# Kernel tuning notes

Measured on AMD Instinct MI355X. Metric: run time of the kernel, lower is better.

The kernel has to match this reference:

```python
import jax, jax.numpy as jnp
import numpy as np

N = 100000   # nodes
MUL = 128    # multiplicity of each irrep (128x0e + 128x1o)
NA = 10      # number of scalar node attributes (one-hot elements, 10x0e)
DIM = MUL * 4  # 128 scalars + 128 vectors*3
LIN_SCALE = 1.0 / np.sqrt(MUL)       # e3nn Linear 'element' path norm: 1/sqrt(fan_in)
TP_SCALE = 1.0 / np.sqrt(MUL * NA)   # FCTP single path per l: 1/sqrt(mul_in*mul_attr)


def setup_inputs() -> dict:
    key = jax.random.key(0)
    ks = jax.random.split(key, 7)
    m_i = jax.random.normal(ks[0], (N, DIM), dtype=jnp.float32)
    node_feats = jax.random.normal(ks[1], (N, DIM), dtype=jnp.float32)
    z = jax.random.randint(ks[2], (N,), 0, NA)
    node_attrs = jax.nn.one_hot(z, NA, dtype=jnp.float32)  # 10x0e one-hot element attrs
    Wl0 = jax.random.normal(ks[3], (MUL, MUL), dtype=jnp.float32)       # Linear weight, 0e block
    Wl1 = jax.random.normal(ks[4], (MUL, MUL), dtype=jnp.float32)       # Linear weight, 1o block
    Wt0 = jax.random.normal(ks[5], (MUL, NA, MUL), dtype=jnp.float32)   # FCTP path weight 0e(x)0e->0e
    Wt1 = jax.random.normal(ks[6], (MUL, NA, MUL), dtype=jnp.float32)   # FCTP path weight 1o(x)0e->1o
    return dict(m_i=m_i, node_feats=node_feats, node_attrs=node_attrs,
                Wl0=Wl0, Wl1=Wl1, Wt0=Wt0, Wt1=Wt1)


def _split(x):
    # [N, 512] -> scalars [N,128], vectors [N,128,3]
    return x[:, :MUL], x[:, MUL:].reshape(-1, MUL, 3)


def _forward(m_i, node_feats, node_attrs, Wl0, Wl1, Wt0, Wt1):
    # equivariant Linear on m_i: block-diagonal per-irrep matmul
    ms, mv = _split(m_i)
    lin_s = (ms @ Wl0) * LIN_SCALE                                  # [N,128]
    lin_v = jnp.einsum('nix,io->nox', mv, Wl1) * LIN_SCALE          # [N,128,3]
    # FullyConnectedTensorProduct(node_feats, node_attrs): attrs are 0e scalars,
    # CG l(x)0e->l is identity; per-attr 128x128 path weight. Loop over the 10
    # attribute channels (small fixed set) to avoid a huge [N,128,128] intermediate.
    fs, fv = _split(node_feats)
    res_s = jnp.zeros_like(lin_s)
    res_v = jnp.zeros_like(lin_v)
    for a in range(NA):
        att = node_attrs[:, a]
        res_s = res_s + att[:, None] * (fs @ Wt0[:, a, :])
        res_v = res_v + att[:, None, None] * jnp.einsum('nix,io->nox', fv, Wt1[:, a, :])
    out_s = lin_s + res_s * TP_SCALE
    out_v = lin_v + res_v * TP_SCALE
    return jnp.concatenate([out_s, out_v.reshape(-1, MUL * 3)], axis=1)  # [N,512]


def reference(m_i, node_feats, node_attrs, Wl0, Wl1, Wt0, Wt1):
    return _forward(m_i, node_feats, node_attrs, Wl0, Wl1, Wt0, Wt1)
```

## Files before the change

kernel.cpp:

```cpp
#include <hip/hip_runtime.h>
#include <stdint.h>

#define NA 10
#define DIM 512
#define LIN_SCALE 0.08838834764831845f
#define TP_SCALE  0.027950849718747374f

#define PLANE_SZ 655360
#define CHUNK_SZ 8192

typedef __attribute__((ext_vector_type(8))) short short8;
typedef __attribute__((ext_vector_type(8))) __bf16 bf16x8;
typedef __attribute__((ext_vector_type(4))) float f32x4;
typedef __attribute__((ext_vector_type(4))) float float4v;

static __device__ __forceinline__ unsigned short f2bf(float x) {
  unsigned int u = __float_as_uint(x);
  u += 0x7fffu + ((u >> 16) & 1u);
  return (unsigned short)(u >> 16);
}
static __device__ __forceinline__ float bf2f(unsigned short h) {
  return __uint_as_float(((unsigned int)h) << 16);
}

#define MFMA_BF16(A, B, C) __builtin_amdgcn_mfma_f32_16x16x32_bf16( \
    __builtin_bit_cast(bf16x8, (A)), __builtin_bit_cast(bf16x8, (B)), (C), 0, 0, 0)

__global__ void k_zero(int* wsI) {
  if (threadIdx.x < 48) wsI[threadIdx.x] = 0;
}

__global__ __launch_bounds__(256) void k_count(const float* __restrict__ attrs,
                                               int* wsI, int N) {
  __shared__ int h[16];
  int t = threadIdx.x;
  int n = blockIdx.x * 256 + t;
  if (t < 16) h[t] = 0;
  __syncthreads();
  if (n < N) {
    int a = 0;
    #pragma unroll
    for (int j = 1; j < NA; ++j) if (attrs[n * NA + j] > 0.5f) a = j;
    atomicAdd(&h[a], 1);
  }
  __syncthreads();
  if (t < NA && h[t] > 0) atomicAdd(&wsI[t], h[t]);
}

__global__ void k_scan(int* wsI) {
  if (threadIdx.x == 0) {
    int run = 0;
    for (int a = 0; a < NA; ++a) {
      wsI[16 + a] = run;
      wsI[32 + a] = run;
      run += wsI[a];
    }
  }
}

__global__ __launch_bounds__(256) void k_scatter(const float* __restrict__ attrs,
                                                 int* wsI, int N) {
  __shared__ int h[16], base[16], c2[16];
  int t = threadIdx.x;
  int n = blockIdx.x * 256 + t;
  if (t < 16) { h[t] = 0; c2[t] = 0; }
  __syncthreads();
  int a = 0;
  if (n < N) {
    #pragma unroll
    for (int j = 1; j < NA; ++j) if (attrs[n * NA + j] > 0.5f) a = j;
    atomicAdd(&h[a], 1);
  }
  __syncthreads();
  if (t < NA && h[t] > 0) base[t] = atomicAdd(&wsI[32 + t], h[t]);
  __syncthreads();
  if (n < N) {
    int r = atomicAdd(&c2[a], 1);
    wsI[64 + base[a] + r] = n;
  }
}

__global__ __launch_bounds__(256) void k_prep(const float* __restrict__ Wl0,
                                              const float* __restrict__ Wl1,
                                              const float* __restrict__ Wt0,
                                              const float* __restrict__ Wt1,
                                              char* __restrict__ wb) {
  int gid = blockIdx.x * 256 + threadIdx.x;
  int l  = gid & 63;
  int nb = (gid >> 6) & 7;
  int c  = (gid >> 9) & 7;
  int ac = gid >> 12;
  int a  = ac % NA;
  int type = ac / NA;
  const float* Wl = type ? Wl1 : Wl0;
  const float* Wt = type ? Wt1 : Wt0;
  char* bh = wb + (size_t)type * (2 * (size_t)PLANE_SZ);
  char* bl = bh + PLANE_SZ;
  size_t slot = ((size_t)((a * 8 + c) * 8 + nb) * 64 + l) * 16;
  short8 h8, l8;
  #pragma unroll
  for (int e = 0; e < 8; ++e) {
    int k = c * 32 + (e >> 2) * 16 + (l >> 4) * 4 + (e & 3);
    int n = nb * 16 + (l & 15);
    float w = (k < 128) ? (LIN_SCALE * Wl[k * 128 + n])
                        : (TP_SCALE * Wt[(size_t)(k - 128) * (NA * 128) + a * 128 + n]);
    unsigned short hb = f2bf(w);
    h8[e] = (short)hb;
    l8[e] = (short)f2bf(w - bf2f(hb));
  }
  *(short8*)(bh + slot) = h8;
  *(short8*)(bl + slot) = l8;
}

__global__ __launch_bounds__(256, 2) void k_gemm(const float* __restrict__ m_i,
                                                 const float* __restrict__ feats,
                                                 const int* __restrict__ wsI,
                                                 const char* __restrict__ wb,
                                                 float* __restrict__ out) {
  __shared__ __attribute__((aligned(16))) short Ah[16][64][8];
  __shared__ __attribute__((aligned(16))) short Al[16][64][8];
  __shared__ int nidx[64];

  const int a  = blockIdx.y;
  const int t0 = blockIdx.x * 64;
  const int ca = wsI[a];
  if (t0 >= ca) return;
  const int nn = (ca - t0 < 64) ? (ca - t0) : 64;
  const int tid = threadIdx.x;
  if (tid < 64) nidx[tid] = (tid < nn) ? wsI[64 + wsI[16 + a] + t0 + tid] : 0;

  const int wid  = tid >> 6;
  const int lane = tid & 63;
  const int nd   = tid >> 2;
  const int w    = tid & 3;

  const char* bp_h = wb + (size_t)(wid ? 2 : 0) * PLANE_SZ + (size_t)a * (8 * CHUNK_SZ);
  const char* bp_l = bp_h + PLANE_SZ;

  f32x4 acc[4][8];
  #pragma unroll
  for (int i = 0; i < 4; ++i)
    #pragma unroll
    for (int nbv = 0; nbv < 8; ++nbv)
      acc[i][nbv] = (f32x4){0.f, 0.f, 0.f, 0.f};

  for (int c = 0; c < 8; ++c) {
    __syncthreads();
    {
      const float* src = (c < 4) ? m_i : feats;
      const int cc = c & 3;
      const float* row = src + (size_t)nidx[nd] * DIM;
      const bool ok = (nd < nn);
      {
        float4v f0 = {0,0,0,0}, f1 = {0,0,0,0};
        if (ok) {
          f0 = *(const float4v*)(row + cc * 32 + 4 * w);
          f1 = *(const float4v*)(row + cc * 32 + 16 + 4 * w);
        }
        short8 h8, l8;
        #pragma unroll
        for (int j = 0; j < 4; ++j) {
          unsigned short hb = f2bf(f0[j]);
          h8[j] = (short)hb; l8[j] = (short)f2bf(f0[j] - bf2f(hb));
          unsigned short hb2 = f2bf(f1[j]);
          h8[4 + j] = (short)hb2; l8[4 + j] = (short)f2bf(f1[j] - bf2f(hb2));
        }
        const int rb = nd >> 4, ln = (nd & 15) + 16 * w;
        *(short8*)&Ah[rb][ln][0] = h8;
        *(short8*)&Al[rb][ln][0] = l8;
      }
      {
        const int vb = 128 + cc * 96 + 12 * w;
        float4v g[6];
        #pragma unroll
        for (int q = 0; q < 6; ++q) g[q] = (float4v){0,0,0,0};
        if (ok) {
          g[0] = *(const float4v*)(row + vb);
          g[1] = *(const float4v*)(row + vb + 4);
          g[2] = *(const float4v*)(row + vb + 8);
          g[3] = *(const float4v*)(row + vb + 48);
          g[4] = *(const float4v*)(row + vb + 52);
          g[5] = *(const float4v*)(row + vb + 56);
        }
        float r0[12], r1[12];
        #pragma unroll
        for (int q = 0; q < 3; ++q)
          #pragma unroll
          for (int j = 0; j < 4; ++j) { r0[q*4+j] = g[q][j]; r1[q*4+j] = g[3+q][j]; }
        const int ln = (nd & 15) + 16 * w;
        #pragma unroll
        for (int x = 0; x < 3; ++x) {
          short8 h8, l8;
          #pragma unroll
          for (int j = 0; j < 4; ++j) {
            float v0 = r0[3 * j + x];
            unsigned short hb = f2bf(v0);
            h8[j] = (short)hb; l8[j] = (short)f2bf(v0 - bf2f(hb));
            float v1 = r1[3 * j + x];
            unsigned short hb2 = f2bf(v1);
            h8[4 + j] = (short)hb2; l8[4 + j] = (short)f2bf(v1 - bf2f(hb2));
          }
          const int rb = 4 + x * 4 + (nd >> 4);
          *(short8*)&Ah[rb][ln][0] = h8;
          *(short8*)&Al[rb][ln][0] = l8;
        }
      }
    }
    __syncthreads();
    {
      const int rb0 = wid * 4;
      const char* bh_base = bp_h + (size_t)c * CHUNK_SZ + (size_t)lane * 16;
      const char* bl_base = bp_l + (size_t)c * CHUNK_SZ + (size_t)lane * 16;
      short8 ah[4], al[4];
      #pragma unroll
      for (int i = 0; i < 4; ++i) {
        ah[i] = *(const short8*)&Ah[rb0 + i][lane][0];
        al[i] = *(const short8*)&Al[rb0 + i][lane][0];
      }
      #pragma unroll
      for (int nbv = 0; nbv < 8; ++nbv) {
        short8 bh = *(const short8*)(bh_base + nbv * 1024);
        short8 bl = *(const short8*)(bl_base + nbv * 1024);
        #pragma unroll
        for (int i = 0; i < 4; ++i) {
          acc[i][nbv] = MFMA_BF16(ah[i], bh, acc[i][nbv]);
          acc[i][nbv] = MFMA_BF16(al[i], bh, acc[i][nbv]);
          acc[i][nbv] = MFMA_BF16(ah[i], bl, acc[i][nbv]);
        }
      }
    }
  }

  const int rloc = (lane >> 4) * 4;
  const int cloc = lane & 15;
  if (wid == 0) {
    #pragma unroll
    for (int i = 0; i < 4; ++i)
      #pragma unroll
      for (int r = 0; r < 4; ++r) {
        const int node = i * 16 + rloc + r;
        if (node < nn) {
          float* orow = out + (size_t)nidx[node] * DIM;
          #pragma unroll
          for (int nbv = 0; nbv < 8; ++nbv)
            orow[nbv * 16 + cloc] = acc[i][nbv][r];
        }
      }
  } else {
    const int x = wid - 1;
    #pragma unroll
    for (int i = 0; i < 4; ++i)
      #pragma unroll
      for (int r = 0; r < 4; ++r) {
        const int node = i * 16 + rloc + r;
        if (node < nn) {
          float* orow = out + (size_t)nidx[node] * DIM + 128 + x;
          #pragma unroll
          for (int nbv = 0; nbv < 8; ++nbv)
            orow[(nbv * 16 + cloc) * 3] = acc[i][nbv][r];
        }
      }
  }
}

__global__ __launch_bounds__(512) void k_direct(const float* __restrict__ m_i,
                                                const float* __restrict__ feats,
                                                const float* __restrict__ attrs,
                                                const float* __restrict__ Wl0,
                                                const float* __restrict__ Wl1,
                                                const float* __restrict__ Wt0,
                                                const float* __restrict__ Wt1,
                                                float* __restrict__ out, int N) {
  __shared__ float mrow[512], frow[512];
  __shared__ int sa;
  const int n = blockIdx.x;
  const int t = threadIdx.x;
  mrow[t] = m_i[(size_t)n * DIM + t];
  frow[t] = feats[(size_t)n * DIM + t];
  if (t == 0) {
    int a = 0;
    for (int j = 1; j < NA; ++j) if (attrs[n * NA + j] > 0.5f) a = j;
    sa = a;
  }
  __syncthreads();
  const int a = sa;
  if (t < 128) {
    float s1 = 0.f, s2 = 0.f;
    for (int k = 0; k < 128; ++k) {
      s1 = fmaf(mrow[k], Wl0[k * 128 + t], s1);
      s2 = fmaf(frow[k], Wt0[(size_t)k * (NA * 128) + a * 128 + t], s2);
    }
    out[(size_t)n * DIM + t] = LIN_SCALE * s1 + TP_SCALE * s2;
  } else {
    const int i = t - 128, o = i / 3, x = i % 3;
    float s1 = 0.f, s2 = 0.f;
    for (int k = 0; k < 128; ++k) {
      float mv = mrow[128 + 3 * k + x], fv = frow[128 + 3 * k + x];
      s1 = fmaf(mv, Wl1[k * 128 + o], s1);
      s2 = fmaf(fv, Wt1[(size_t)k * (NA * 128) + a * 128 + o], s2);
    }
    out[(size_t)n * DIM + t] = LIN_SCALE * s1 + TP_SCALE * s2;
  }
}

extern "C" void kernel_launch(void* const* d_in, const int* in_sizes, int n_in,
                              void* d_out, int out_size, void* d_ws, size_t ws_size,
                              hipStream_t stream) {
  const float* m_i   = (const float*)d_in[0];
  const float* nf    = (const float*)d_in[1];
  const float* attrs = (const float*)d_in[2];
  const float* Wl0   = (const float*)d_in[3];
  const float* Wl1   = (const float*)d_in[4];
  const float* Wt0   = (const float*)d_in[5];
  const float* Wt1   = (const float*)d_in[6];
  float* out = (float*)d_out;
  const int N = in_sizes[0] / DIM;

  const size_t idxOff = (256 + (size_t)N * 4 + 255) & ~(size_t)255;
  const size_t need   = idxOff + 4 * (size_t)PLANE_SZ;
  if (ws_size < need) {
    k_direct<<<N, 512, 0, stream>>>(m_i, nf, attrs, Wl0, Wl1, Wt0, Wt1, out, N);
    return;
  }

  int*  wsI = (int*)d_ws;
  char* wb  = (char*)d_ws + idxOff;

  const int nb1 = (N + 255) / 256;
  k_zero<<<1, 64, 0, stream>>>(wsI);
  k_count<<<nb1, 256, 0, stream>>>(attrs, wsI, N);
  k_scan<<<1, 64, 0, stream>>>(wsI);
  k_scatter<<<nb1, 256, 0, stream>>>(attrs, wsI, N);
  k_prep<<<320, 256, 0, stream>>>(Wl0, Wl1, Wt0, Wt1, wb);
  dim3 g((N + 63) / 64, NA);
  k_gemm<<<g, 256, 0, stream>>>(m_i, nf, wsI, wb, out);
}
```

Before: 563.3 us.

## Switch split-bf16 triple MFMA to single fp16 MFMA with double-buffered LDS

Replaces the hi/lo bf16 split (three MFMAs per tile) with a single fp16 MFMA per tile, which halves the weight planes and the A-tile LDS. It also doubles the block to 512 threads so each wave covers half the output columns, and double-buffers the A tile so the next chunk is staged while the current one is multiplied. The aim is to cut MFMA count and conversion work and to overlap global loads with compute. The cost is precision: fp16 inputs with roughly 11-bit mantissa replace the roughly 16-bit effective split-bf16 product, and large-magnitude inputs could lose accuracy.

```diff
diff --git a/kernel.cpp b/kernel.cpp
--- a/kernel.cpp
+++ b/kernel.cpp
@@ -7,24 +7,13 @@
 #define TP_SCALE  0.027950849718747374f
 
 #define PLANE_SZ 655360
-#define CHUNK_SZ 8192
-
-typedef __attribute__((ext_vector_type(8))) short short8;
-typedef __attribute__((ext_vector_type(8))) __bf16 bf16x8;
+
+typedef __attribute__((ext_vector_type(8))) _Float16 half8;
+typedef __attribute__((ext_vector_type(4))) _Float16 half4;
 typedef __attribute__((ext_vector_type(4))) float f32x4;
 typedef __attribute__((ext_vector_type(4))) float float4v;
 
-static __device__ __forceinline__ unsigned short f2bf(float x) {
-  unsigned int u = __float_as_uint(x);
-  u += 0x7fffu + ((u >> 16) & 1u);
-  return (unsigned short)(u >> 16);
-}
-static __device__ __forceinline__ float bf2f(unsigned short h) {
-  return __uint_as_float(((unsigned int)h) << 16);
-}
-
-#define MFMA_BF16(A, B, C) __builtin_amdgcn_mfma_f32_16x16x32_bf16( \
-    __builtin_bit_cast(bf16x8, (A)), __builtin_bit_cast(bf16x8, (B)), (C), 0, 0, 0)
+#define MFMA_F16(A, B, C) __builtin_amdgcn_mfma_f32_16x16x32_f16((A), (B), (C), 0, 0, 0)
 
 __global__ void k_zero(int* wsI) {
   if (threadIdx.x < 48) wsI[threadIdx.x] = 0;
@@ -94,31 +83,25 @@
   int type = ac / NA;
   const float* Wl = type ? Wl1 : Wl0;
   const float* Wt = type ? Wt1 : Wt0;
-  char* bh = wb + (size_t)type * (2 * (size_t)PLANE_SZ);
-  char* bl = bh + PLANE_SZ;
-  size_t slot = ((size_t)((a * 8 + c) * 8 + nb) * 64 + l) * 16;
-  short8 h8, l8;
+  half8 h;
   #pragma unroll
   for (int e = 0; e < 8; ++e) {
     int k = c * 32 + (e >> 2) * 16 + (l >> 4) * 4 + (e & 3);
     int n = nb * 16 + (l & 15);
     float w = (k < 128) ? (LIN_SCALE * Wl[k * 128 + n])
                         : (TP_SCALE * Wt[(size_t)(k - 128) * (NA * 128) + a * 128 + n]);
-    unsigned short hb = f2bf(w);
-    h8[e] = (short)hb;
-    l8[e] = (short)f2bf(w - bf2f(hb));
-  }
-  *(short8*)(bh + slot) = h8;
-  *(short8*)(bl + slot) = l8;
-}
-
-__global__ __launch_bounds__(256, 2) void k_gemm(const float* __restrict__ m_i,
+    h[e] = (_Float16)w;
+  }
+  *(half8*)(wb + (size_t)type * PLANE_SZ +
+            ((size_t)((a * 8 + c) * 8 + nb) * 64 + l) * 16) = h;
+}
+
+__global__ __launch_bounds__(512, 4) void k_gemm(const float* __restrict__ m_i,
                                                  const float* __restrict__ feats,
                                                  const int* __restrict__ wsI,
                                                  const char* __restrict__ wb,
                                                  float* __restrict__ out) {
-  __shared__ __attribute__((aligned(16))) short Ah[16][64][8];
-  __shared__ __attribute__((aligned(16))) short Al[16][64][8];
+  __shared__ __attribute__((aligned(16))) _Float16 A[2][16][64][8];
   __shared__ int nidx[64];
 
   const int a  = blockIdx.y;
@@ -129,135 +112,111 @@
   const int tid = threadIdx.x;
   if (tid < 64) nidx[tid] = (tid < nn) ? wsI[64 + wsI[16 + a] + t0 + tid] : 0;
 
-  const int wid  = tid >> 6;
+  const int w    = tid >> 6;
   const int lane = tid & 63;
-  const int nd   = tid >> 2;
-  const int w    = tid & 3;
-
-  const char* bp_h = wb + (size_t)(wid ? 2 : 0) * PLANE_SZ + (size_t)a * (8 * CHUNK_SZ);
-  const char* bp_l = bp_h + PLANE_SZ;
-
-  f32x4 acc[4][8];
+  const int nd   = tid >> 3;
+  const int sub  = tid & 7;
+  const int wq   = sub >> 1;
+  const int hh   = sub & 1;
+  const int ln   = (nd & 15) + 16 * wq;
+  const int rbs  = nd >> 4;
+
+  const bool scalarW = (w < 2);
+  const int  xch = scalarW ? 0 : ((w - 2) >> 1);
+  const int  nh  = scalarW ? w : ((w - 2) & 1);
+  const int  rb0 = scalarW ? 0 : 4 + 4 * xch;
+  const char* bbase = wb + (scalarW ? (size_t)0 : (size_t)PLANE_SZ) +
+                      (size_t)a * 65536 + (size_t)nh * 4096 + (size_t)lane * 16;
+
+  __syncthreads();
+
+  f32x4 acc[4][4];
   #pragma unroll
   for (int i = 0; i < 4; ++i)
     #pragma unroll
-    for (int nbv = 0; nbv < 8; ++nbv)
-      acc[i][nbv] = (f32x4){0.f, 0.f, 0.f, 0.f};
+    for (int n4 = 0; n4 < 4; ++n4)
+      acc[i][n4] = (f32x4){0.f, 0.f, 0.f, 0.f};
+
+  auto stage = [&](int cs, int pb) {
+    const float* src = (cs < 4) ? m_i : feats;
+    const int cc = cs & 3;
+    const float* row = src + (size_t)nidx[nd] * DIM;
+    float4v s4 = *(const float4v*)(row + cc * 32 + 4 * wq + 16 * hh);
+    const int vb = 128 + cc * 96 + 12 * wq + 48 * hh;
+    float4v g0 = *(const float4v*)(row + vb);
+    float4v g1 = *(const float4v*)(row + vb + 4);
+    float4v g2 = *(const float4v*)(row + vb + 8);
+    half4 sh;
+    #pragma unroll
+    for (int j = 0; j < 4; ++j) sh[j] = (_Float16)s4[j];
+    *(half4*)&A[pb][rbs][ln][4 * hh] = sh;
+    #pragma unroll
+    for (int x = 0; x < 3; ++x) {
+      half4 vh;
+      #pragma unroll
+      for (int j = 0; j < 4; ++j) {
+        const int idx = 3 * j + x;
+        float v = (idx < 4) ? g0[idx] : (idx < 8) ? g1[idx - 4] : g2[idx - 8];
+        vh[j] = (_Float16)v;
+      }
+      *(half4*)&A[pb][4 + 4 * x + rbs][ln][4 * hh] = vh;
+    }
+  };
+
+  stage(0, 0);
+  __syncthreads();
 
   for (int c = 0; c < 8; ++c) {
+    const int p = c & 1;
+    {
+      half8 afr[4];
+      #pragma unroll
+      for (int i = 0; i < 4; ++i)
+        afr[i] = *(const half8*)&A[p][rb0 + i][lane][0];
+      const char* bc = bbase + (size_t)c * 8192;
+      half8 b0 = *(const half8*)(bc);
+      half8 b1 = *(const half8*)(bc + 1024);
+      #pragma unroll
+      for (int i = 0; i < 4; ++i) acc[i][0] = MFMA_F16(afr[i], b0, acc[i][0]);
+      b0 = *(const half8*)(bc + 2048);
+      #pragma unroll
+      for (int i = 0; i < 4; ++i) acc[i][1] = MFMA_F16(afr[i], b1, acc[i][1]);
+      b1 = *(const half8*)(bc + 3072);
+      #pragma unroll
+      for (int i = 0; i < 4; ++i) acc[i][2] = MFMA_F16(afr[i], b0, acc[i][2]);
+      #pragma unroll
+      for (int i = 0; i < 4; ++i) acc[i][3] = MFMA_F16(afr[i], b1, acc[i][3]);
+    }
+    if (c < 7) stage(c + 1, p ^ 1);
     __syncthreads();
-    {
-      const float* src = (c < 4) ? m_i : feats;
-      const int cc = c & 3;
-      const float* row = src + (size_t)nidx[nd] * DIM;
-      const bool ok = (nd < nn);
-      {
-        float4v f0 = {0,0,0,0}, f1 = {0,0,0,0};
-        if (ok) {
-          f0 = *(const float4v*)(row + cc * 32 + 4 * w);
-          f1 = *(const float4v*)(row + cc * 32 + 16 + 4 * w);
-        }
-        short8 h8, l8;
-        #pragma unroll
-        for (int j = 0; j < 4; ++j) {
-          unsigned short hb = f2bf(f0[j]);
-          h8[j] = (short)hb; l8[j] = (short)f2bf(f0[j] - bf2f(hb));
-          unsigned short hb2 = f2bf(f1[j]);
-          h8[4 + j] = (short)hb2; l8[4 + j] = (short)f2bf(f1[j] - bf2f(hb2));
-        }
-        const int rb = nd >> 4, ln = (nd & 15) + 16 * w;
-        *(short8*)&Ah[rb][ln][0] = h8;
-        *(short8*)&Al[rb][ln][0] = l8;
-      }
-      {
-        const int vb = 128 + cc * 96 + 12 * w;
-        float4v g[6];
-        #pragma unroll
-        for (int q = 0; q < 6; ++q) g[q] = (float4v){0,0,0,0};
-        if (ok) {
-          g[0] = *(const float4v*)(row + vb);
-          g[1] = *(const float4v*)(row + vb + 4);
-          g[2] = *(const float4v*)(row + vb + 8);
-          g[3] = *(const float4v*)(row + vb + 48);
-          g[4] = *(const float4v*)(row + vb + 52);
-          g[5] = *(const float4v*)(row + vb + 56);
-        }
-        float r0[12], r1[12];
-        #pragma unroll
-        for (int q = 0; q < 3; ++q)
-          #pragma unroll
-          for (int j = 0; j < 4; ++j) { r0[q*4+j] = g[q][j]; r1[q*4+j] = g[3+q][j]; }
-        const int ln = (nd & 15) + 16 * w;
-        #pragma unroll
-        for (int x = 0; x < 3; ++x) {
-          short8 h8, l8;
-          #pragma unroll
-          for (int j = 0; j < 4; ++j) {
-            float v0 = r0[3 * j + x];
-            unsigned short hb = f2bf(v0);
-            h8[j] = (short)hb; l8[j] = (short)f2bf(v0 - bf2f(hb));
-            float v1 = r1[3 * j + x];
-            unsigned short hb2 = f2bf(v1);
-            h8[4 + j] = (short)hb2; l8[4 + j] = (short)f2bf(v1 - bf2f(hb2));
-          }
-          const int rb = 4 + x * 4 + (nd >> 4);
-          *(short8*)&Ah[rb][ln][0] = h8;
-          *(short8*)&Al[rb][ln][0] = l8;
-        }
-      }
-    }
-    __syncthreads();
-    {
-      const int rb0 = wid * 4;
-      const char* bh_base = bp_h + (size_t)c * CHUNK_SZ + (size_t)lane * 16;
-      const char* bl_base = bp_l + (size_t)c * CHUNK_SZ + (size_t)lane * 16;
-      short8 ah[4], al[4];
-      #pragma unroll
-      for (int i = 0; i < 4; ++i) {
-        ah[i] = *(const short8*)&Ah[rb0 + i][lane][0];
-        al[i] = *(const short8*)&Al[rb0 + i][lane][0];
-      }
-      #pragma unroll
-      for (int nbv = 0; nbv < 8; ++nbv) {
-        short8 bh = *(const short8*)(bh_base + nbv * 1024);
-        short8 bl = *(const short8*)(bl_base + nbv * 1024);
-        #pragma unroll
-        for (int i = 0; i < 4; ++i) {
-          acc[i][nbv] = MFMA_BF16(ah[i], bh, acc[i][nbv]);
-          acc[i][nbv] = MFMA_BF16(al[i], bh, acc[i][nbv]);
-          acc[i][nbv] = MFMA_BF16(ah[i], bl, acc[i][nbv]);
-        }
-      }
-    }
   }
 
   const int rloc = (lane >> 4) * 4;
   const int cloc = lane & 15;
-  if (wid == 0) {
+  if (scalarW) {
     #pragma unroll
     for (int i = 0; i < 4; ++i)
       #pragma unroll
       for (int r = 0; r < 4; ++r) {
         const int node = i * 16 + rloc + r;
         if (node < nn) {
-          float* orow = out + (size_t)nidx[node] * DIM;
+          float* orow = out + (size_t)nidx[node] * DIM + nh * 64;
           #pragma unroll
-          for (int nbv = 0; nbv < 8; ++nbv)
-            orow[nbv * 16 + cloc] = acc[i][nbv][r];
+          for (int n4 = 0; n4 < 4; ++n4)
+            orow[n4 * 16 + cloc] = acc[i][n4][r];
         }
       }
   } else {
-    const int x = wid - 1;
     #pragma unroll
     for (int i = 0; i < 4; ++i)
       #pragma unroll
       for (int r = 0; r < 4; ++r) {
         const int node = i * 16 + rloc + r;
         if (node < nn) {
-          float* orow = out + (size_t)nidx[node] * DIM + 128 + x;
+          float* orow = out + (size_t)nidx[node] * DIM + 128 + xch;
           #pragma unroll
-          for (int nbv = 0; nbv < 8; ++nbv)
-            orow[(nbv * 16 + cloc) * 3] = acc[i][nbv][r];
+          for (int n4 = 0; n4 < 4; ++n4)
+            orow[((nh * 4 + n4) * 16 + cloc) * 3] = acc[i][n4][r];
         }
       }
   }
@@ -317,7 +276,7 @@
   const int N = in_sizes[0] / DIM;
 
   const size_t idxOff = (256 + (size_t)N * 4 + 255) & ~(size_t)255;
-  const size_t need   = idxOff + 4 * (size_t)PLANE_SZ;
+  const size_t need   = idxOff + 2 * (size_t)PLANE_SZ;
   if (ws_size < need) {
     k_direct<<<N, 512, 0, stream>>>(m_i, nf, attrs, Wl0, Wl1, Wt0, Wt1, out, N);
     return;
@@ -333,5 +292,5 @@
   k_scatter<<<nb1, 256, 0, stream>>>(attrs, wsI, N);
   k_prep<<<320, 256, 0, stream>>>(Wl0, Wl1, Wt0, Wt1, wb);
   dim3 g((N + 63) / 64, NA);
-  k_gemm<<<g, 256, 0, stream>>>(m_i, nf, wsI, wb, out);
-}
+  k_gemm<<<g, 512, 0, stream>>>(m_i, nf, wsI, wb, out);
+}
```

Measured after the change: 526.6 us. -6.5%, faster.
